# Performance work log

Measured on AMD Instinct MI355X. Metric: run time of the kernel, lower is better.

## Reference

```python
import jax, jax.numpy as jnp
import numpy as np

N_NODES = 50000
N_EDGES = 800000
IN_F = 256
OUT_F = 64
N_HEADS = 8
LRELU_SLOPE = 0.2


def setup_inputs() -> dict:
    key = jax.random.key(0)
    ks = jax.random.split(key, 6)
    x = jax.random.normal(ks[0], (N_NODES, IN_F), dtype=jnp.float32)
    src = jax.random.randint(ks[1], (N_EDGES,), 0, N_NODES, dtype=jnp.int32)
    dst = jax.random.randint(ks[2], (N_EDGES,), 0, N_NODES, dtype=jnp.int32)
    M_values = jax.random.uniform(ks[3], (N_EDGES,), dtype=jnp.float32)
    # xavier_uniform-ish scale (gain=1.414)
    wscale = 1.414 * np.sqrt(6.0 / (IN_F + OUT_F))
    W = jax.random.uniform(ks[4], (N_HEADS, IN_F, OUT_F), dtype=jnp.float32,
                           minval=-wscale, maxval=wscale)
    ascale = 1.414 * np.sqrt(6.0 / (OUT_F + 1))
    a = jax.random.uniform(ks[5], (N_HEADS, 2, OUT_F), dtype=jnp.float32,
                           minval=-ascale, maxval=ascale)
    return {"x": x, "src": src, "dst": dst, "M_values": M_values, "W": W, "a": a}


def reference(x, src, dst, M_values, W, a):
    # x: [N, Fin]; src/dst: [E]; M_values: [E] (edge-aligned mask/weights)
    # W: [H, Fin, Fout]; a: [H, 2, Fout] (a[:,0]=a_self, a[:,1]=a_neighs)
    N = x.shape[0]
    outs = []
    for hidx in range(W.shape[0]):  # small fixed head count
        h = x @ W[hidx]                       # [N, Fout]
        a_self = h @ a[hidx, 0]               # [N]
        a_neigh = h @ a[hidx, 1]              # [N]
        e = jax.nn.leaky_relu(a_self[src] + a_neigh[dst], LRELU_SLOPE) * M_values  # [E]
        exp_e = jnp.exp(e)
        denom = jax.ops.segment_sum(exp_e, dst, num_segments=N)   # [N]
        att = exp_e / (denom[dst] + 1e-16)                        # [E]
        h_prime = jax.ops.segment_sum(att[:, None] * h[src], dst, num_segments=N)  # [N, Fout]
        outs.append(jax.nn.elu(h_prime))      # concat=True -> elu per head
    return jnp.concatenate(outs, axis=1)       # [N, H*Fout]
```

## Files before the change

kernel.cpp:

```cpp
#include <hip/hip_runtime.h>
#include <math.h>

#define N_NODES 50000
#define N_EDGES 800000
#define IN_F 256
#define OUT_F 64
#define N_HEADS 8
#define SLOPE 0.2f

typedef __attribute__((ext_vector_type(8))) __bf16 bf16x8;
typedef __attribute__((ext_vector_type(4))) __bf16 bf16x4;
typedef __attribute__((ext_vector_type(4))) float floatx4;
typedef __attribute__((ext_vector_type(4))) float f32x4;
typedef __attribute__((ext_vector_type(2))) int i32x2;
typedef __attribute__((ext_vector_type(2))) unsigned int u32x2;
typedef __attribute__((ext_vector_type(8))) char schar8;

#define HIST_BLOCKS   3125
#define CAST_W_BLOCKS 512
#define PREP_BLOCKS   (HIST_BLOCKS + CAST_W_BLOCKS)

__global__ __launch_bounds__(256) void prep_kernel(const float* __restrict__ W,
                                                   const int* __restrict__ dst,
                                                   __bf16* __restrict__ Wt,
                                                   int* __restrict__ deg) {
    const int b = blockIdx.x;
    const int t = threadIdx.x;
    if (b < HIST_BLOCKS) {
        int e = b * 256 + t;
        atomicAdd(&deg[dst[e]], 1);
    } else {
        int i = (b - HIST_BLOCKS) * 256 + t;
        int n = i & (OUT_F - 1);
        int k = (i >> 6) & (IN_F - 1);
        int h = i >> 14;
        Wt[((size_t)h * OUT_F + n) * IN_F + k] = (__bf16)W[i];
    }
}

#define XPAD 264
__global__ __launch_bounds__(256) void mfma_gemm_kernel(const float* __restrict__ x,
                                                        const __bf16* __restrict__ Wt,
                                                        const float* __restrict__ a,
                                                        unsigned char* __restrict__ hb,
                                                        float2* __restrict__ asc,
                                                        float* __restrict__ a_neigh) {
    __shared__ __bf16 xs[32][XPAD];
    const int warp = threadIdx.x >> 6;
    const int tile = blockIdx.x;
    const int n0 = tile * 32;
    const int lane = threadIdx.x & 63;
    const int l15 = lane & 15;
    const int quad = lane >> 4;
    const int h0 = warp * 2;

#pragma unroll
    for (int i = 0; i < 8; i++) {
        int c4 = i * 256 + threadIdx.x;
        int row = c4 >> 6;
        int col = (c4 & 63) * 4;
        int node = n0 + row;
        node = (node < N_NODES) ? node : (N_NODES - 1);
        f32x4 v = __builtin_nontemporal_load((const f32x4*)x + (size_t)node * 64 + (c4 & 63));
        bf16x4 o;
        o[0] = (__bf16)v[0]; o[1] = (__bf16)v[1]; o[2] = (__bf16)v[2]; o[3] = (__bf16)v[3];
        *(bf16x4*)&xs[row][col] = o;
    }
    __syncthreads();

    floatx4 acc[2][2][4];
#pragma unroll
    for (int hh = 0; hh < 2; hh++)
#pragma unroll
        for (int i = 0; i < 2; i++)
#pragma unroll
            for (int c = 0; c < 4; c++) acc[hh][i][c] = floatx4{0.f, 0.f, 0.f, 0.f};

    const __bf16* wb0 = Wt + ((size_t)h0 * OUT_F + l15) * IN_F + quad * 8;
    const __bf16* wb1 = wb0 + (size_t)OUT_F * IN_F;

#pragma unroll
    for (int k0 = 0; k0 < IN_F; k0 += 32) {
        bf16x8 a0 = *(const bf16x8*)&xs[l15][k0 + quad * 8];
        bf16x8 a1 = *(const bf16x8*)&xs[l15 + 16][k0 + quad * 8];
#pragma unroll
        for (int c = 0; c < 4; c++) {
            bf16x8 b0 = *(const bf16x8*)(wb0 + (size_t)c * 16 * IN_F + k0);
            acc[0][0][c] = __builtin_amdgcn_mfma_f32_16x16x32_bf16(a0, b0, acc[0][0][c], 0, 0, 0);
            acc[0][1][c] = __builtin_amdgcn_mfma_f32_16x16x32_bf16(a1, b0, acc[0][1][c], 0, 0, 0);
            bf16x8 b1 = *(const bf16x8*)(wb1 + (size_t)c * 16 * IN_F + k0);
            acc[1][0][c] = __builtin_amdgcn_mfma_f32_16x16x32_bf16(a0, b1, acc[1][0][c], 0, 0, 0);
            acc[1][1][c] = __builtin_amdgcn_mfma_f32_16x16x32_bf16(a1, b1, acc[1][1][c], 0, 0, 0);
        }
    }

    __syncthreads();
    char* myc = (char*)xs + warp * (32 * OUT_F);

#pragma unroll
    for (int hh = 0; hh < 2; hh++) {
        const int head = h0 + hh;
        float av0[4], av1[4];
#pragma unroll
        for (int c = 0; c < 4; c++) {
            av0[c] = a[head * 2 * OUT_F + c * 16 + l15];
            av1[c] = a[head * 2 * OUT_F + OUT_F + c * 16 + l15];
        }
#pragma unroll
        for (int i = 0; i < 2; i++) {
#pragma unroll
            for (int reg = 0; reg < 4; reg++) {
                float ps = 0.f, pn = 0.f, rm = 0.f;
#pragma unroll
                for (int c = 0; c < 4; c++) {
                    float v = acc[hh][i][c][reg];
                    ps = fmaf(v, av0[c], ps);
                    pn = fmaf(v, av1[c], pn);
                    rm = fmaxf(rm, fabsf(v));
                }
#pragma unroll
                for (int off = 1; off < 16; off <<= 1) {
                    ps += __shfl_xor(ps, off, 64);
                    pn += __shfl_xor(pn, off, 64);
                    rm = fmaxf(rm, __shfl_xor(rm, off, 64));
                }
                const float inv = (rm > 0.f) ? 127.f / rm : 0.f;
                const int rowoff = (i * 16 + quad * 4 + reg) * OUT_F;
#pragma unroll
                for (int c = 0; c < 4; c++) {
                    float q = rintf(acc[hh][i][c][reg] * inv);
                    q = fminf(fmaxf(q, -127.f), 127.f);
                    myc[rowoff + c * 16 + l15] = (char)((int)q + 128);
                }
                int node = n0 + i * 16 + quad * 4 + reg;
                if (l15 == 0 && node < N_NODES) {
                    asc[node * N_HEADS + head] = make_float2(ps, rm * (1.f / 127.f));
                    a_neigh[node * N_HEADS + head] = pn;
                }
            }
        }
#pragma unroll
        for (int pass = 0; pass < 4; pass++) {
            int row = pass * 8 + (lane >> 3);
            int node = n0 + row;
            schar8 v = *(const schar8*)&myc[row * OUT_F + (lane & 7) * 8];
            if (node < N_NODES)
                *(schar8*)(hb + ((size_t)(node * N_HEADS + head) << 6) + (lane & 7) * 8) = v;
        }
    }
}

#define SB 512
#define NSB 98
__global__ void scanA(const int* __restrict__ deg, int* __restrict__ start,
                      int* __restrict__ bsum) {
    __shared__ int tmp[SB];
    int t = threadIdx.x, i = blockIdx.x * SB + t;
    int v = (i < N_NODES) ? deg[i] : 0;
    tmp[t] = v;
    for (int off = 1; off < SB; off <<= 1) {
        __syncthreads();
        int add = (t >= off) ? tmp[t - off] : 0;
        __syncthreads();
        tmp[t] += add;
    }
    if (i < N_NODES) start[i] = tmp[t] - v;
    if (t == SB - 1) bsum[blockIdx.x] = tmp[SB - 1];
}

__global__ void scanC(int* __restrict__ start, const int* __restrict__ bsum,
                      int* __restrict__ cursor) {
    __shared__ int pre[128];
    int t = threadIdx.x;
    if (t < 128) pre[t] = (t < NSB) ? bsum[t] : 0;
    __syncthreads();
    for (int off = 1; off < 128; off <<= 1) {
        int add = (t < 128 && t >= off) ? pre[t - off] : 0;
        __syncthreads();
        if (t < 128) pre[t] += add;
        __syncthreads();
    }
    int excl = (blockIdx.x == 0) ? 0 : pre[blockIdx.x - 1];
    int i = blockIdx.x * SB + t;
    if (i < N_NODES) {
        int s = start[i] + excl;
        start[i] = s;
        cursor[i] = s;
    }
}

__global__ void fill_kernel(const int* __restrict__ src, const int* __restrict__ dst,
                            const float* __restrict__ M, int* __restrict__ cursor,
                            i32x2* __restrict__ csr_sm) {
    int e = blockIdx.x * 256 + threadIdx.x;
    if (e < N_EDGES) {
        int d = dst[e];
        int pos = atomicAdd(&cursor[d], 1);
        i32x2 v;
        v.x = src[e];
        v.y = __float_as_int(M[e] * 1.44269504f);
        __builtin_nontemporal_store(v, csr_sm + pos);
    }
}

__global__ __launch_bounds__(256) void agg_kernel(const unsigned char* __restrict__ hb,
                                                  const float2* __restrict__ asc,
                                                  const float* __restrict__ a_neigh,
                                                  const int* __restrict__ start,
                                                  const int* __restrict__ deg,
                                                  const i32x2* __restrict__ csr_sm,
                                                  float* __restrict__ out) {
    int n = blockIdx.x * 4 + (threadIdx.x >> 6);
    if (n >= N_NODES) return;
    const int lane = threadIdx.x & 63;
    const int head = lane >> 3;

    const int d = deg[n];
    float* ob = &out[((size_t)n << 9) + (lane << 3)];
    if (d == 0) {
        f32x4 z = {0.f, 0.f, 0.f, 0.f};
        *(f32x4*)(ob) = z;
        *(f32x4*)(ob + 4) = z;
        return;
    }
    const int dm1 = d - 1;
    const float an = a_neigh[(n << 3) + head];
    const unsigned char* hbl = hb + (lane << 3);
    const float2* aslc = asc + head;
    const i32x2* cp = csr_sm + start[n];

    float facc[8];
#pragma unroll
    for (int k = 0; k < 8; k++) facc[k] = 0.f;
    float den = 0.f, sacc = 0.f;

    auto edge = [&](const i32x2& sm, const float2& a2, const u32x2& hv) {
        float e_ = a2.x + an;
        e_ = (e_ > 0.f) ? e_ : SLOPE * e_;
        const float w_ = exp2f(e_ * __int_as_float(sm.y));
        const float ws = w_ * a2.y;
        den += w_;
        sacc += ws;
        facc[0] = fmaf(ws, (float)(hv.x & 0xffu), facc[0]);
        facc[1] = fmaf(ws, (float)((hv.x >> 8) & 0xffu), facc[1]);
        facc[2] = fmaf(ws, (float)((hv.x >> 16) & 0xffu), facc[2]);
        facc[3] = fmaf(ws, (float)(hv.x >> 24), facc[3]);
        facc[4] = fmaf(ws, (float)(hv.y & 0xffu), facc[4]);
        facc[5] = fmaf(ws, (float)((hv.y >> 8) & 0xffu), facc[5]);
        facc[6] = fmaf(ws, (float)((hv.y >> 16) & 0xffu), facc[6]);
        facc[7] = fmaf(ws, (float)(hv.y >> 24), facc[7]);
    };

    i32x2 smP = cp[0];
    float2 aP = aslc[(size_t)smP.x << 3];
    u32x2 hvP = *(const u32x2*)(hbl + ((size_t)smP.x << 9));

    int j = 0;
    for (; j + 2 <= d; j += 2) {
        i32x2 smQ = cp[j + 1];
        float2 aQ = aslc[(size_t)smQ.x << 3];
        u32x2 hvQ = *(const u32x2*)(hbl + ((size_t)smQ.x << 9));
        edge(smP, aP, hvP);
        int i2 = (j + 2 < d) ? (j + 2) : dm1;
        smP = cp[i2];
        aP = aslc[(size_t)smP.x << 3];
        hvP = *(const u32x2*)(hbl + ((size_t)smP.x << 9));
        edge(smQ, aQ, hvQ);
    }
    if (j < d) edge(smP, aP, hvP);

    const float inv = 1.f / (den + 1e-16f);
    float r[8];
#pragma unroll
    for (int k = 0; k < 8; k++) {
        float v = fmaf(-128.f, sacc, facc[k]) * inv;
        r[k] = (v > 0.f) ? v : expm1f(v);
    }
    *(float4*)(ob)     = make_float4(r[0], r[1], r[2], r[3]);
    *(float4*)(ob + 4) = make_float4(r[4], r[5], r[6], r[7]);
}

extern "C" void kernel_launch(void* const* d_in, const int* in_sizes, int n_in,
                              void* d_out, int out_size, void* d_ws, size_t ws_size,
                              hipStream_t stream) {
    const float* x   = (const float*)d_in[0];
    const int*   src = (const int*)d_in[1];
    const int*   dst = (const int*)d_in[2];
    const float* M   = (const float*)d_in[3];
    const float* W   = (const float*)d_in[4];
    const float* a   = (const float*)d_in[5];
    float* out = (float*)d_out;

    char* p = (char*)d_ws;
    auto alloc = [&](size_t bytes) {
        char* r = p;
        p += (bytes + 255) & ~(size_t)255;
        return r;
    };
    unsigned char* hb = (unsigned char*)alloc((size_t)N_NODES * N_HEADS * OUT_F);
    float2* asc     = (float2*)alloc(sizeof(float2) * N_NODES * N_HEADS);
    float*  a_neigh = (float*)alloc(sizeof(float) * N_NODES * N_HEADS);
    int*    deg     = (int*)alloc(sizeof(int) * N_NODES);
    int*    start   = (int*)alloc(sizeof(int) * N_NODES);
    int*    cursor  = (int*)alloc(sizeof(int) * N_NODES);
    int*    bsum    = (int*)alloc(sizeof(int) * 256);
    i32x2*  csr_sm  = (i32x2*)alloc(sizeof(i32x2) * N_EDGES);
    __bf16* Wt      = (__bf16*)alloc(sizeof(__bf16) * N_HEADS * IN_F * OUT_F);

    hipMemsetAsync(deg, 0, sizeof(int) * N_NODES, stream);
    prep_kernel<<<PREP_BLOCKS, 256, 0, stream>>>(W, dst, Wt, deg);

    scanA<<<NSB, SB, 0, stream>>>(deg, start, bsum);
    scanC<<<NSB, SB, 0, stream>>>(start, bsum, cursor);
    fill_kernel<<<(N_EDGES + 255) / 256, 256, 0, stream>>>(src, dst, M, cursor, csr_sm);

    mfma_gemm_kernel<<<1563, 256, 0, stream>>>(x, Wt, a, hb, asc, a_neigh);

    agg_kernel<<<(N_NODES + 3) / 4, 256, 0, stream>>>(hb, asc, a_neigh,
                                                      start, deg, csr_sm, out);
}
```

Baseline: 401.3 us.

## Merge scan into single block, fuse CSR fill into GEMM, widen aggregation blocks

```diff
diff --git a/kernel.cpp b/kernel.cpp
--- a/kernel.cpp
+++ b/kernel.cpp
@@ -38,17 +38,67 @@
     }
 }
 
+#define CHUNK 49
+__global__ __launch_bounds__(1024) void scan_kernel(const int* __restrict__ deg,
+                                                    int* __restrict__ cursor,
+                                                    i32x2* __restrict__ sd) {
+    __shared__ int sums[1024];
+    const int t = threadIdx.x;
+    const int c0 = t * CHUNK;
+    int local = 0;
+    for (int i = 0; i < CHUNK; i++) {
+        int idx = c0 + i;
+        local += (idx < N_NODES) ? deg[idx] : 0;
+    }
+    sums[t] = local;
+    __syncthreads();
+    for (int off = 1; off < 1024; off <<= 1) {
+        int add = (t >= off) ? sums[t - off] : 0;
+        __syncthreads();
+        sums[t] += add;
+        __syncthreads();
+    }
+    int run = (t == 0) ? 0 : sums[t - 1];
+    for (int i = 0; i < CHUNK; i++) {
+        int idx = c0 + i;
+        if (idx < N_NODES) {
+            int dv = deg[idx];
+            cursor[idx] = run;
+            i32x2 v; v.x = run; v.y = dv;
+            sd[idx] = v;
+            run += dv;
+        }
+    }
+}
+
+#define GEMM_BLOCKS 1563
+#define GF_BLOCKS   4688
 #define XPAD 264
-__global__ __launch_bounds__(256) void mfma_gemm_kernel(const float* __restrict__ x,
-                                                        const __bf16* __restrict__ Wt,
-                                                        const float* __restrict__ a,
-                                                        unsigned char* __restrict__ hb,
-                                                        float2* __restrict__ asc,
-                                                        float* __restrict__ a_neigh) {
+__global__ __launch_bounds__(256) void gemm_fill_kernel(
+        const float* __restrict__ x, const __bf16* __restrict__ Wt,
+        const float* __restrict__ a, unsigned char* __restrict__ hb,
+        float2* __restrict__ asc, float* __restrict__ a_neigh,
+        const int* __restrict__ src, const int* __restrict__ dst,
+        const float* __restrict__ M, int* __restrict__ cursor,
+        i32x2* __restrict__ csr_sm) {
     __shared__ __bf16 xs[32][XPAD];
+    const int b = blockIdx.x;
+    const int g = b / 3;
+    if ((b % 3) != 0) {
+        int fb = b - (b + 2) / 3;
+        int e = fb * 256 + threadIdx.x;
+        if (e < N_EDGES) {
+            int d = dst[e];
+            int pos = atomicAdd(&cursor[d], 1);
+            i32x2 v;
+            v.x = src[e];
+            v.y = __float_as_int(M[e] * 1.44269504f);
+            __builtin_nontemporal_store(v, csr_sm + pos);
+        }
+        return;
+    }
     const int warp = threadIdx.x >> 6;
-    const int tile = blockIdx.x;
-    const int n0 = tile * 32;
+    const int n0 = g * 32;
     const int lane = threadIdx.x & 63;
     const int l15 = lane & 15;
     const int quad = lane >> 4;
@@ -150,72 +200,18 @@
     }
 }
 
-#define SB 512
-#define NSB 98
-__global__ void scanA(const int* __restrict__ deg, int* __restrict__ start,
-                      int* __restrict__ bsum) {
-    __shared__ int tmp[SB];
-    int t = threadIdx.x, i = blockIdx.x * SB + t;
-    int v = (i < N_NODES) ? deg[i] : 0;
-    tmp[t] = v;
-    for (int off = 1; off < SB; off <<= 1) {
-        __syncthreads();
-        int add = (t >= off) ? tmp[t - off] : 0;
-        __syncthreads();
-        tmp[t] += add;
-    }
-    if (i < N_NODES) start[i] = tmp[t] - v;
-    if (t == SB - 1) bsum[blockIdx.x] = tmp[SB - 1];
-}
-
-__global__ void scanC(int* __restrict__ start, const int* __restrict__ bsum,
-                      int* __restrict__ cursor) {
-    __shared__ int pre[128];
-    int t = threadIdx.x;
-    if (t < 128) pre[t] = (t < NSB) ? bsum[t] : 0;
-    __syncthreads();
-    for (int off = 1; off < 128; off <<= 1) {
-        int add = (t < 128 && t >= off) ? pre[t - off] : 0;
-        __syncthreads();
-        if (t < 128) pre[t] += add;
-        __syncthreads();
-    }
-    int excl = (blockIdx.x == 0) ? 0 : pre[blockIdx.x - 1];
-    int i = blockIdx.x * SB + t;
-    if (i < N_NODES) {
-        int s = start[i] + excl;
-        start[i] = s;
-        cursor[i] = s;
-    }
-}
-
-__global__ void fill_kernel(const int* __restrict__ src, const int* __restrict__ dst,
-                            const float* __restrict__ M, int* __restrict__ cursor,
-                            i32x2* __restrict__ csr_sm) {
-    int e = blockIdx.x * 256 + threadIdx.x;
-    if (e < N_EDGES) {
-        int d = dst[e];
-        int pos = atomicAdd(&cursor[d], 1);
-        i32x2 v;
-        v.x = src[e];
-        v.y = __float_as_int(M[e] * 1.44269504f);
-        __builtin_nontemporal_store(v, csr_sm + pos);
-    }
-}
-
-__global__ __launch_bounds__(256) void agg_kernel(const unsigned char* __restrict__ hb,
+__global__ __launch_bounds__(512) void agg_kernel(const unsigned char* __restrict__ hb,
                                                   const float2* __restrict__ asc,
                                                   const float* __restrict__ a_neigh,
-                                                  const int* __restrict__ start,
-                                                  const int* __restrict__ deg,
+                                                  const i32x2* __restrict__ sd,
                                                   const i32x2* __restrict__ csr_sm,
                                                   float* __restrict__ out) {
-    int n = blockIdx.x * 4 + (threadIdx.x >> 6);
-    if (n >= N_NODES) return;
+    int n = blockIdx.x * 8 + (threadIdx.x >> 6);
     const int lane = threadIdx.x & 63;
     const int head = lane >> 3;
 
-    const int d = deg[n];
+    i32x2 sdv = sd[n];
+    const int d = sdv.y;
     float* ob = &out[((size_t)n << 9) + (lane << 3)];
     if (d == 0) {
         f32x4 z = {0.f, 0.f, 0.f, 0.f};
@@ -225,9 +221,11 @@
     }
     const int dm1 = d - 1;
     const float an = a_neigh[(n << 3) + head];
-    const unsigned char* hbl = hb + (lane << 3);
-    const float2* aslc = asc + head;
-    const i32x2* cp = csr_sm + start[n];
+    const char* hbB = (const char*)hb;
+    const char* ascB = (const char*)asc;
+    const unsigned int loff = (unsigned)lane << 3;
+    const unsigned int hoff = (unsigned)head << 3;
+    const i32x2* cp = csr_sm + sdv.x;
 
     float facc[8];
 #pragma unroll
@@ -235,8 +233,8 @@
     float den = 0.f, sacc = 0.f;
 
     auto edge = [&](const i32x2& sm, const float2& a2, const u32x2& hv) {
-        float e_ = a2.x + an;
-        e_ = (e_ > 0.f) ? e_ : SLOPE * e_;
+        float s = a2.x + an;
+        float e_ = fmaxf(s, SLOPE * s);
         const float w_ = exp2f(e_ * __int_as_float(sm.y));
         const float ws = w_ * a2.y;
         den += w_;
@@ -252,19 +250,19 @@
     };
 
     i32x2 smP = cp[0];
-    float2 aP = aslc[(size_t)smP.x << 3];
-    u32x2 hvP = *(const u32x2*)(hbl + ((size_t)smP.x << 9));
+    float2 aP = *(const float2*)(ascB + (((unsigned)smP.x << 6) | hoff));
+    u32x2 hvP = *(const u32x2*)(hbB + (((unsigned)smP.x << 9) | loff));
 
     int j = 0;
     for (; j + 2 <= d; j += 2) {
         i32x2 smQ = cp[j + 1];
-        float2 aQ = aslc[(size_t)smQ.x << 3];
-        u32x2 hvQ = *(const u32x2*)(hbl + ((size_t)smQ.x << 9));
+        float2 aQ = *(const float2*)(ascB + (((unsigned)smQ.x << 6) | hoff));
+        u32x2 hvQ = *(const u32x2*)(hbB + (((unsigned)smQ.x << 9) | loff));
         edge(smP, aP, hvP);
         int i2 = (j + 2 < d) ? (j + 2) : dm1;
         smP = cp[i2];
-        aP = aslc[(size_t)smP.x << 3];
-        hvP = *(const u32x2*)(hbl + ((size_t)smP.x << 9));
+        aP = *(const float2*)(ascB + (((unsigned)smP.x << 6) | hoff));
+        hvP = *(const u32x2*)(hbB + (((unsigned)smP.x << 9) | loff));
         edge(smQ, aQ, hvQ);
     }
     if (j < d) edge(smP, aP, hvP);
@@ -301,21 +299,18 @@
     float2* asc     = (float2*)alloc(sizeof(float2) * N_NODES * N_HEADS);
     float*  a_neigh = (float*)alloc(sizeof(float) * N_NODES * N_HEADS);
     int*    deg     = (int*)alloc(sizeof(int) * N_NODES);
-    int*    start   = (int*)alloc(sizeof(int) * N_NODES);
     int*    cursor  = (int*)alloc(sizeof(int) * N_NODES);
-    int*    bsum    = (int*)alloc(sizeof(int) * 256);
+    i32x2*  sd      = (i32x2*)alloc(sizeof(i32x2) * N_NODES);
     i32x2*  csr_sm  = (i32x2*)alloc(sizeof(i32x2) * N_EDGES);
     __bf16* Wt      = (__bf16*)alloc(sizeof(__bf16) * N_HEADS * IN_F * OUT_F);
 
     hipMemsetAsync(deg, 0, sizeof(int) * N_NODES, stream);
     prep_kernel<<<PREP_BLOCKS, 256, 0, stream>>>(W, dst, Wt, deg);
 
-    scanA<<<NSB, SB, 0, stream>>>(deg, start, bsum);
-    scanC<<<NSB, SB, 0, stream>>>(start, bsum, cursor);
-    fill_kernel<<<(N_EDGES + 255) / 256, 256, 0, stream>>>(src, dst, M, cursor, csr_sm);
-
-    mfma_gemm_kernel<<<1563, 256, 0, stream>>>(x, Wt, a, hb, asc, a_neigh);
-
-    agg_kernel<<<(N_NODES + 3) / 4, 256, 0, stream>>>(hb, asc, a_neigh,
-                                                      start, deg, csr_sm, out);
-}
+    scan_kernel<<<1, 1024, 0, stream>>>(deg, cursor, sd);
+
+    gemm_fill_kernel<<<GF_BLOCKS, 256, 0, stream>>>(x, Wt, a, hb, asc, a_neigh,
+                                                    src, dst, M, cursor, csr_sm);
+
+    agg_kernel<<<6250, 512, 0, stream>>>(hb, asc, a_neigh, sd, csr_sm, out);
+}
```

Measured after the change: 486.7 us. 1.21x slower.
